# Performance work log

Hardware: AMD Instinct MI355X
Metric: run time of the kernel (lower is better)

## Reference

```python
import jax, jax.numpy as jnp
import numpy as np

N = 50000   # nodes
E = 800000  # edges
IN, HID, OUT = 128, 128, 64


def setup_inputs() -> dict:
    key = jax.random.key(0)
    ks = jax.random.split(key, 16)
    x = jax.random.normal(ks[0], (N, IN), dtype=jnp.float32)
    src = jax.random.randint(ks[1], (E,), 0, N, dtype=jnp.int32)
    dst = jax.random.randint(ks[2], (E,), 0, N, dtype=jnp.int32)
    s = 1.0 / np.sqrt(IN)
    W_self1 = jax.random.normal(ks[3], (IN, HID), dtype=jnp.float32) * s
    W_neigh1 = jax.random.normal(ks[4], (IN, HID), dtype=jnp.float32) * s
    b1 = jnp.zeros((HID,), dtype=jnp.float32)
    W_self2 = jax.random.normal(ks[5], (HID, HID), dtype=jnp.float32) * s
    W_neigh2 = jax.random.normal(ks[6], (HID, HID), dtype=jnp.float32) * s
    b2 = jnp.zeros((HID,), dtype=jnp.float32)
    W_self3 = jax.random.normal(ks[7], (HID, OUT), dtype=jnp.float32) * s
    W_neigh3 = jax.random.normal(ks[8], (HID, OUT), dtype=jnp.float32) * s
    b3 = jnp.zeros((OUT,), dtype=jnp.float32)
    # dropout(p=0.5) masks, pre-scaled by 1/(1-p)
    keep = 0.5
    mask1 = (jax.random.uniform(ks[9], (N, HID)) < keep).astype(jnp.float32) / keep
    mask2 = (jax.random.uniform(ks[10], (N, HID)) < keep).astype(jnp.float32) / keep
    return dict(x=x, src=src, dst=dst,
                W_self1=W_self1, W_neigh1=W_neigh1, b1=b1,
                W_self2=W_self2, W_neigh2=W_neigh2, b2=b2,
                W_self3=W_self3, W_neigh3=W_neigh3, b3=b3,
                mask1=mask1, mask2=mask2)


def _mean_agg(h, src, dst):
    # gather source features, segment-sum into destinations, divide by in-degree
    summed = jax.ops.segment_sum(h[src], dst, num_segments=N)  # [N, d]
    deg = jax.ops.segment_sum(jnp.ones((E,), dtype=h.dtype), dst, num_segments=N)
    return summed / jnp.maximum(deg, 1.0)[:, None]


def _sage_layer(h, src, dst, W_self, W_neigh, b):
    h_neigh = _mean_agg(h, src, dst)
    return h @ W_self + h_neigh @ W_neigh + b


def reference(x, src, dst, W_self1, W_neigh1, b1, W_self2, W_neigh2, b2,
              W_self3, W_neigh3, b3, mask1, mask2):
    h = _sage_layer(x, src, dst, W_self1, W_neigh1, b1)
    h = jax.nn.relu(h) * mask1
    h = _sage_layer(h, src, dst, W_self2, W_neigh2, b2)
    h = jax.nn.relu(h) * mask2
    h = _sage_layer(h, src, dst, W_self3, W_neigh3, b3)
    return h
```

## Files before the change

### kernel.cpp

```cpp
#include <hip/hip_runtime.h>
#include <hip/hip_bf16.h>

#define DIN  128
#define DHID 128
#define DOUT 64

#define EB   4096
#define CAPB 5120

typedef short short8 __attribute__((ext_vector_type(8)));
typedef float f32x4  __attribute__((ext_vector_type(4)));

__device__ __forceinline__ ushort f2bf(float f) {
    union { float f; uint u; } c; c.f = f;
    uint u = c.u;
    return (ushort)((u + 0x7fff + ((u >> 16) & 1)) >> 16);
}
__device__ __forceinline__ float bf2f(uint h16) {
    union { uint u; float f; } c; c.u = h16 << 16;
    return c.f;
}
__device__ __forceinline__ float sb8(uint u, int k) {
    return (float)((int)(u << (24 - 8 * k)) >> 24);
}

__device__ __forceinline__ void wprep_dev(const float* __restrict__ W,
                                          ushort* __restrict__ Wt, int OUT, int idx) {
    int nn = idx >> 7;
    int k  = idx & 127;
    Wt[idx] = f2bf(W[(size_t)k * OUT + nn]);
}

__global__ __launch_bounds__(256)
void megaprep(const int* __restrict__ src, const int* __restrict__ dst, int E, int fillB,
              int* __restrict__ bkt_cur, uint* __restrict__ pairs,
              const float* __restrict__ x, ushort* __restrict__ xb, int n4, int cvtB,
              const float* __restrict__ Ws1, const float* __restrict__ Wn1,
              const float* __restrict__ Ws2, const float* __restrict__ Wn2,
              const float* __restrict__ Ws3, const float* __restrict__ Wn3,
              ushort* __restrict__ Wst1, ushort* __restrict__ Wnt1,
              ushort* __restrict__ Wst2, ushort* __restrict__ Wnt2,
              ushort* __restrict__ Wst3, ushort* __restrict__ Wnt3) {
    __shared__ int c[256];
    __shared__ int startl[256];
    __shared__ int ofs[256];
    int b = blockIdx.x;
    const int t = threadIdx.x;
    if (b < fillB) {
        c[t] = 0;
        __syncthreads();
        const int base = b * EB;
        const int end = min(base + EB, E);
        for (int i = base + t; i < end; i += 256)
            atomicAdd(&c[dst[i] >> 8], 1);
        __syncthreads();
        int v = c[t];
        startl[t] = v ? (t * CAPB + atomicAdd(&bkt_cur[t], v)) : 0;
        ofs[t] = 0;
        __syncthreads();
        for (int i = base + t; i < end; i += 256) {
            int d = dst[i];
            int bb = d >> 8;
            int p = startl[bb] + atomicAdd(&ofs[bb], 1);
            pairs[p] = ((uint)src[i] << 8) | (uint)(d & 255);
        }
        return;
    }
    b -= fillB;
    if (b < cvtB) {
        int i = b * 256 + t;
        if (i < n4) {
            float4 v = ((const float4*)x)[i];
            ushort4 o;
            o.x = f2bf(v.x); o.y = f2bf(v.y); o.z = f2bf(v.z); o.w = f2bf(v.w);
            ((ushort4*)xb)[i] = o;
        }
        return;
    }
    b -= cvtB;
    if (b < 64)  { wprep_dev(Ws1, Wst1, 128, b * 256 + t); return; }
    b -= 64;
    if (b < 64)  { wprep_dev(Wn1, Wnt1, 128, b * 256 + t); return; }
    b -= 64;
    if (b < 64)  { wprep_dev(Ws2, Wst2, 128, b * 256 + t); return; }
    b -= 64;
    if (b < 64)  { wprep_dev(Wn2, Wnt2, 128, b * 256 + t); return; }
    b -= 64;
    if (b < 32)  { wprep_dev(Ws3, Wst3, 64, b * 256 + t); return; }
    b -= 32;
    wprep_dev(Wn3, Wnt3, 64, b * 256 + t);
}

__global__ __launch_bounds__(256)
void bucket_csr(const uint* __restrict__ pairs, const int* __restrict__ bkt_cur,
                int* __restrict__ row_ptr, int* __restrict__ deg,
                int* __restrict__ esrc, int N, int nbkt) {
    constexpr int CAP = 6144;
    __shared__ uint pl[CAP];
    __shared__ int cnt[256];
    __shared__ int rs[256];
    __shared__ int sc[256];
    const int bkt = blockIdx.x;
    const int t = threadIdx.x;
    const int ebase = bkt * CAPB;
    const int ecnt  = min(bkt_cur[bkt], CAPB);
    cnt[t] = 0;
    __syncthreads();
    const bool fits = (ecnt <= CAP);
    if (fits) {
        for (int i = t; i < ecnt; i += 256) {
            uint p = pairs[ebase + i];
            pl[i] = p;
            atomicAdd(&cnt[p & 255u], 1);
        }
    } else {
        for (int i = t; i < ecnt; i += 256)
            atomicAdd(&cnt[pairs[ebase + i] & 255u], 1);
    }
    __syncthreads();
    int own = cnt[t];
    sc[t] = own;
    __syncthreads();
    for (int o = 1; o < 256; o <<= 1) {
        int u = (t >= o) ? sc[t - o] : 0;
        __syncthreads();
        sc[t] += u;
        __syncthreads();
    }
    rs[t] = sc[t] - own;
    const int node = bkt * 256 + t;
    if (node < N) {
        row_ptr[node] = ebase + rs[t];
        deg[node] = own;
    }
    __syncthreads();
    if (fits) {
        for (int i = t; i < ecnt; i += 256) {
            uint p = pl[i];
            int pos = atomicAdd(&rs[p & 255u], 1);
            esrc[ebase + pos] = (int)(p >> 8);
        }
    } else {
        for (int i = t; i < ecnt; i += 256) {
            uint p = pairs[ebase + i];
            int pos = atomicAdd(&rs[p & 255u], 1);
            esrc[ebase + pos] = (int)(p >> 8);
        }
    }
}

template<int OUTW>
__global__ __launch_bounds__(256)
void sage_gemm(const ushort* __restrict__ Hb,
               const ushort* __restrict__ Wst,
               const ushort* __restrict__ Wnt,
               ushort* __restrict__ S,
               signed char* __restrict__ Gq,
               float* __restrict__ Gsc,
               int n) {
    constexpr int NT = OUTW / 16;
    __shared__ ushort Wl[2][OUTW * 128];

    const int tid  = threadIdx.x;
    const int lane = tid & 63;
    const int wave = tid >> 6;
    const int rg   = wave >> 1;
    const int isG  = wave & 1;
    const int m16  = lane & 15;
    const int kb   = lane >> 4;
    const int rbase = blockIdx.x * 64 + rg * 32;

    {
        const uint4* s4 = (const uint4*)Wst;
        const uint4* n4 = (const uint4*)Wnt;
        uint4* ls = (uint4*)&Wl[0][0];
        uint4* ln = (uint4*)&Wl[1][0];
#pragma unroll
        for (int j = tid; j < OUTW * 128 / 8; j += 256) {
            ls[j] = s4[j];
            ln[j] = n4[j];
        }
    }

    short8 a[2][4];
#pragma unroll
    for (int mt = 0; mt < 2; ++mt) {
        int arow = rbase + mt * 16 + m16;
        if (arow >= n) arow = n - 1;
        const ushort* __restrict__ Ap = &Hb[(size_t)arow * 128 + kb * 8];
#pragma unroll
        for (int c = 0; c < 4; ++c)
            a[mt][c] = *(const short8*)(Ap + c * 32);
    }

    __syncthreads();

    f32x4 acc[2][NT];
#pragma unroll
    for (int mt = 0; mt < 2; ++mt)
#pragma unroll
        for (int t = 0; t < NT; ++t) acc[mt][t] = (f32x4)(0.f);

    const ushort* __restrict__ Wp = &Wl[isG][0];
#pragma unroll
    for (int t = 0; t < NT; ++t) {
#pragma unroll
        for (int c = 0; c < 4; ++c) {
            short8 b = *(const short8*)&Wp[(t * 16 + m16) * 128 + c * 32 + kb * 8];
            acc[0][t] = __builtin_amdgcn_mfma_f32_16x16x32_bf16(a[0][c], b, acc[0][t], 0, 0, 0);
            acc[1][t] = __builtin_amdgcn_mfma_f32_16x16x32_bf16(a[1][c], b, acc[1][t], 0, 0, 0);
        }
    }

#pragma unroll
    for (int mt = 0; mt < 2; ++mt) {
        const int rb = rbase + mt * 16;
        if (!isG) {
#pragma unroll
            for (int r = 0; r < 4; ++r) {
                int row = rb + kb * 4 + r;
                if (row >= n) continue;
#pragma unroll
                for (int t = 0; t < NT; ++t)
                    S[(size_t)row * OUTW + t * 16 + m16] = f2bf(acc[mt][t][r]);
            }
        } else {
#pragma unroll
            for (int r = 0; r < 4; ++r) {
                float mx = 0.f;
#pragma unroll
                for (int t = 0; t < NT; ++t) mx = fmaxf(mx, fabsf(acc[mt][t][r]));
                mx = fmaxf(mx, __shfl_xor(mx, 1));
                mx = fmaxf(mx, __shfl_xor(mx, 2));
                mx = fmaxf(mx, __shfl_xor(mx, 4));
                mx = fmaxf(mx, __shfl_xor(mx, 8));
                int row = rb + kb * 4 + r;
                if (row >= n) continue;
                float inv = (mx > 0.f) ? 127.f / mx : 0.f;
                if (m16 == 0) Gsc[row] = mx * (1.f / 127.f);
#pragma unroll
                for (int t = 0; t < NT; ++t) {
                    int q = (int)rintf(acc[mt][t][r] * inv);
                    q = max(-127, min(127, q));
                    Gq[(size_t)row * OUTW + t * 16 + m16] = (signed char)q;
                }
            }
        }
    }
}

__device__ __forceinline__ void acc8(float* af, uint2 v, float sc) {
    af[0] += sc * sb8(v.x, 0); af[1] += sc * sb8(v.x, 1);
    af[2] += sc * sb8(v.x, 2); af[3] += sc * sb8(v.x, 3);
    af[4] += sc * sb8(v.y, 0); af[5] += sc * sb8(v.y, 1);
    af[6] += sc * sb8(v.y, 2); af[7] += sc * sb8(v.y, 3);
}
__device__ __forceinline__ void acc4(float* af, uint v, float sc) {
    af[0] += sc * sb8(v, 0); af[1] += sc * sb8(v, 1);
    af[2] += sc * sb8(v, 2); af[3] += sc * sb8(v, 3);
}

#define SPAN_CAP 1024

template<bool FINAL>
__global__ __launch_bounds__(256)
void sage_gather(const signed char* __restrict__ Gq, const float* __restrict__ Gsc,
                 const ushort* __restrict__ S, const float* __restrict__ bias,
                 const float* __restrict__ mask,
                 const int* __restrict__ row_ptr, const int* __restrict__ deg,
                 const int* __restrict__ esrc,
                 void* __restrict__ outv, int n) {
    constexpr int OUTW = FINAL ? 64 : 128;
    __shared__ int   idx_s[SPAN_CAP];
    __shared__ float sc_s[SPAN_CAP];

    const int tid  = threadIdx.x;
    const int lane = tid & 63;
    const int wave = tid >> 6;
    const int qw   = lane >> 4;
    const int l16  = lane & 15;
    const int base = blockIdx.x * 32;

    const int last   = min(base + 31, n - 1);
    const int span_s = row_ptr[base];
    const int span_e = row_ptr[last] + deg[last];
    const int len    = span_e - span_s;
    const bool staged = (len <= SPAN_CAP);
    if (staged) {
        for (int i = tid; i < len; i += 256) {
            int s_ = esrc[span_s + i];
            idx_s[i] = s_;
            sc_s[i] = Gsc[s_];
        }
    }
    __syncthreads();

#pragma unroll
    for (int j = 0; j < 2; ++j) {
        const int node = base + (wave * 4 + qw) * 2 + j;
        if (node >= n) continue;
        const int d = deg[node];
        const float inv = 1.f / fmaxf((float)d, 1.f);

        float af[8] = {0.f, 0.f, 0.f, 0.f, 0.f, 0.f, 0.f, 0.f};
        if (!FINAL) {
            const signed char* __restrict__ gp = Gq + l16 * 8;
            if (staged) {
                int i = row_ptr[node] - span_s, e = i + d;
                for (; i + 7 < e; i += 8) {
                    uint2 v[8]; float c[8];
#pragma unroll
                    for (int k = 0; k < 8; ++k) {
                        int ns = idx_s[i + k];
                        v[k] = *(const uint2*)&gp[(size_t)ns * 128];
                        c[k] = sc_s[i + k];
                    }
#pragma unroll
                    for (int k = 0; k < 8; ++k) acc8(af, v[k], c[k]);
                }
                for (; i < e; ++i) {
                    int ns = idx_s[i];
                    acc8(af, *(const uint2*)&gp[(size_t)ns * 128], sc_s[i]);
                }
            } else {
                int i = row_ptr[node], e = i + d;
                for (; i < e; ++i) {
                    int ns = esrc[i];
                    acc8(af, *(const uint2*)&gp[(size_t)ns * 128], Gsc[ns]);
                }
            }
            const int col0 = l16 * 8;
            uint4 sv = *(const uint4*)&S[(size_t)node * 128 + col0];
            float4 b0 = *(const float4*)&bias[col0];
            float4 b1 = *(const float4*)&bias[col0 + 4];
            float z[8];
            z[0] = bf2f(sv.x & 0xffffu) + af[0] * inv + b0.x;
            z[1] = bf2f(sv.x >> 16)     + af[1] * inv + b0.y;
            z[2] = bf2f(sv.y & 0xffffu) + af[2] * inv + b0.z;
            z[3] = bf2f(sv.y >> 16)     + af[3] * inv + b0.w;
            z[4] = bf2f(sv.z & 0xffffu) + af[4] * inv + b1.x;
            z[5] = bf2f(sv.z >> 16)     + af[5] * inv + b1.y;
            z[6] = bf2f(sv.w & 0xffffu) + af[6] * inv + b1.z;
            z[7] = bf2f(sv.w >> 16)     + af[7] * inv + b1.w;
            float4 m0 = *(const float4*)&mask[(size_t)node * 128 + col0];
            float4 m1 = *(const float4*)&mask[(size_t)node * 128 + col0 + 4];
            z[0] = fmaxf(z[0], 0.f) * m0.x; z[1] = fmaxf(z[1], 0.f) * m0.y;
            z[2] = fmaxf(z[2], 0.f) * m0.z; z[3] = fmaxf(z[3], 0.f) * m0.w;
            z[4] = fmaxf(z[4], 0.f) * m1.x; z[5] = fmaxf(z[5], 0.f) * m1.y;
            z[6] = fmaxf(z[6], 0.f) * m1.z; z[7] = fmaxf(z[7], 0.f) * m1.w;
            uint4 pk;
            pk.x = (uint)f2bf(z[0]) | ((uint)f2bf(z[1]) << 16);
            pk.y = (uint)f2bf(z[2]) | ((uint)f2bf(z[3]) << 16);
            pk.z = (uint)f2bf(z[4]) | ((uint)f2bf(z[5]) << 16);
            pk.w = (uint)f2bf(z[6]) | ((uint)f2bf(z[7]) << 16);
            *(uint4*)&((ushort*)outv)[(size_t)node * 128 + col0] = pk;
        } else {
            const signed char* __restrict__ gp = Gq + l16 * 4;
            if (staged) {
                int i = row_ptr[node] - span_s, e = i + d;
                for (; i + 7 < e; i += 8) {
                    uint v[8]; float c[8];
#pragma unroll
                    for (int k = 0; k < 8; ++k) {
                        int ns = idx_s[i + k];
                        v[k] = *(const uint*)&gp[(size_t)ns * 64];
                        c[k] = sc_s[i + k];
                    }
#pragma unroll
                    for (int k = 0; k < 8; ++k) acc4(af, v[k], c[k]);
                }
                for (; i < e; ++i) {
                    int ns = idx_s[i];
                    acc4(af, *(const uint*)&gp[(size_t)ns * 64], sc_s[i]);
                }
            } else {
                int i = row_ptr[node], e = i + d;
                for (; i < e; ++i) {
                    int ns = esrc[i];
                    acc4(af, *(const uint*)&gp[(size_t)ns * 64], Gsc[ns]);
                }
            }
            const int col0 = l16 * 4;
            uint2 sv = *(const uint2*)&S[(size_t)node * 64 + col0];
            float4 b0 = *(const float4*)&bias[col0];
            float4 z;
            z.x = bf2f(sv.x & 0xffffu) + af[0] * inv + b0.x;
            z.y = bf2f(sv.x >> 16)     + af[1] * inv + b0.y;
            z.z = bf2f(sv.y & 0xffffu) + af[2] * inv + b0.z;
            z.w = bf2f(sv.y >> 16)     + af[3] * inv + b0.w;
            *(float4*)&((float*)outv)[(size_t)node * 64 + col0] = z;
        }
    }
}

extern "C" void kernel_launch(void* const* d_in, const int* in_sizes, int n_in,
                              void* d_out, int out_size, void* d_ws, size_t ws_size,
                              hipStream_t stream) {
    const float* x   = (const float*)d_in[0];
    const int*   src = (const int*)d_in[1];
    const int*   dst = (const int*)d_in[2];
    const float* Ws1 = (const float*)d_in[3];
    const float* Wn1 = (const float*)d_in[4];
    const float* b1  = (const float*)d_in[5];
    const float* Ws2 = (const float*)d_in[6];
    const float* Wn2 = (const float*)d_in[7];
    const float* b2  = (const float*)d_in[8];
    const float* Ws3 = (const float*)d_in[9];
    const float* Wn3 = (const float*)d_in[10];
    const float* b3  = (const float*)d_in[11];
    const float* mask1 = (const float*)d_in[12];
    const float* mask2 = (const float*)d_in[13];
    float* out = (float*)d_out;

    const int N = in_sizes[0] / DIN;
    const int E = in_sizes[1];
    const int nbkt = (N + 255) >> 8;

    char* ws = (char*)d_ws;
    int* bkt_cur  = (int*)ws;
    int* row_ptr  = bkt_cur + 256;
    int* deg      = row_ptr + N;
    int* esrc     = deg + N;
    size_t off = ((size_t)(256 + 2 * N + nbkt * CAPB) * sizeof(int) + 255) & ~(size_t)255;
    uint* pairs  = (uint*)(ws + off);    off += (size_t)nbkt * CAPB * 4;
    ushort* xb   = (ushort*)(ws + off);  off += (size_t)N * 128 * 2;
    ushort* h1b  = (ushort*)(ws + off);  off += (size_t)N * 128 * 2;
    ushort* h2b  = (ushort*)(ws + off);  off += (size_t)N * 128 * 2;
    ushort* S    = (ushort*)(ws + off);  off += (size_t)N * 128 * 2;
    signed char* Gq = (signed char*)(ws + off); off += (size_t)N * 128;
    float* Gsc   = (float*)(ws + off);   off += (size_t)N * 4;
    ushort* Wst1 = (ushort*)(ws + off);  off += 128 * 128 * 2;
    ushort* Wnt1 = (ushort*)(ws + off);  off += 128 * 128 * 2;
    ushort* Wst2 = (ushort*)(ws + off);  off += 128 * 128 * 2;
    ushort* Wnt2 = (ushort*)(ws + off);  off += 128 * 128 * 2;
    ushort* Wst3 = (ushort*)(ws + off);  off += 64 * 128 * 2;
    ushort* Wnt3 = (ushort*)(ws + off);  off += 64 * 128 * 2;

    const int n4 = N * 128 / 4;
    const int cvtB = (n4 + 255) / 256;
    const int fillB = (E + EB - 1) / EB;

    hipMemsetAsync(bkt_cur, 0, 256 * sizeof(int), stream);
    megaprep<<<fillB + cvtB + 4 * 64 + 2 * 32, 256, 0, stream>>>(
        src, dst, E, fillB, bkt_cur, pairs,
        x, xb, n4, cvtB,
        Ws1, Wn1, Ws2, Wn2, Ws3, Wn3,
        Wst1, Wnt1, Wst2, Wnt2, Wst3, Wnt3);

    bucket_csr<<<nbkt, 256, 0, stream>>>(pairs, bkt_cur, row_ptr, deg, esrc, N, nbkt);

    const int gemmB = (N + 63) / 64;
    const int gathB = (N + 31) / 32;

    sage_gemm<128><<<gemmB, 256, 0, stream>>>(xb, Wst1, Wnt1, S, Gq, Gsc, N);
    sage_gather<false><<<gathB, 256, 0, stream>>>(Gq, Gsc, S, b1, mask1, row_ptr, deg, esrc, h1b, N);
    sage_gemm<128><<<gemmB, 256, 0, stream>>>(h1b, Wst2, Wnt2, S, Gq, Gsc, N);
    sage_gather<false><<<gathB, 256, 0, stream>>>(Gq, Gsc, S, b2, mask2, row_ptr, deg, esrc, h2b, N);
    sage_gemm<64><<<gemmB, 256, 0, stream>>>(h2b, Wst3, Wnt3, S, Gq, Gsc, N);
    sage_gather<true><<<gathB, 256, 0, stream>>>(Gq, Gsc, S, b3, nullptr, row_ptr, deg, esrc, out, N);
}
```

Baseline: 296.5 us.

## Fuse self-term GEMM into gather kernel and drop bf16 S buffer round trip

The self projection h@W_self moves from the GEMM kernel into the gather kernel. Each gather block computes its 32 rows with MFMA into shared-memory float tiles, so the separate S buffer is no longer written and re-read through global memory. The GEMM kernel now computes only the neighbor projection and its int8 quantization, one 16-row tile per wave. The self term is now kept in fp32 instead of rounded to bf16. The trade-off is more shared memory and extra weight loads per gather block, which may lower occupancy. The bucket_csr kernel also drops its fallback path for oversized buckets and always stages pairs in shared memory.

```diff
diff --git a/kernel.cpp b/kernel.cpp
--- a/kernel.cpp
+++ b/kernel.cpp
@@ -106,16 +106,10 @@
     const int ecnt  = min(bkt_cur[bkt], CAPB);
     cnt[t] = 0;
     __syncthreads();
-    const bool fits = (ecnt <= CAP);
-    if (fits) {
-        for (int i = t; i < ecnt; i += 256) {
-            uint p = pairs[ebase + i];
-            pl[i] = p;
-            atomicAdd(&cnt[p & 255u], 1);
-        }
-    } else {
-        for (int i = t; i < ecnt; i += 256)
-            atomicAdd(&cnt[pairs[ebase + i] & 255u], 1);
+    for (int i = t; i < ecnt; i += 256) {
+        uint p = pairs[ebase + i];
+        pl[i] = p;
+        atomicAdd(&cnt[p & 255u], 1);
     }
     __syncthreads();
     int own = cnt[t];
@@ -134,117 +128,80 @@
         deg[node] = own;
     }
     __syncthreads();
-    if (fits) {
-        for (int i = t; i < ecnt; i += 256) {
-            uint p = pl[i];
-            int pos = atomicAdd(&rs[p & 255u], 1);
-            esrc[ebase + pos] = (int)(p >> 8);
-        }
-    } else {
-        for (int i = t; i < ecnt; i += 256) {
-            uint p = pairs[ebase + i];
-            int pos = atomicAdd(&rs[p & 255u], 1);
-            esrc[ebase + pos] = (int)(p >> 8);
-        }
+    for (int i = t; i < ecnt; i += 256) {
+        uint p = pl[i];
+        int pos = atomicAdd(&rs[p & 255u], 1);
+        esrc[ebase + pos] = (int)(p >> 8);
     }
 }
 
 template<int OUTW>
 __global__ __launch_bounds__(256)
-void sage_gemm(const ushort* __restrict__ Hb,
-               const ushort* __restrict__ Wst,
-               const ushort* __restrict__ Wnt,
-               ushort* __restrict__ S,
-               signed char* __restrict__ Gq,
-               float* __restrict__ Gsc,
-               int n) {
+void gemm_G(const ushort* __restrict__ Hb,
+            const ushort* __restrict__ Wnt,
+            signed char* __restrict__ Gq,
+            float* __restrict__ Gsc,
+            int n) {
     constexpr int NT = OUTW / 16;
-    __shared__ ushort Wl[2][OUTW * 128];
+    __shared__ ushort Wl[OUTW * 128];
 
     const int tid  = threadIdx.x;
     const int lane = tid & 63;
     const int wave = tid >> 6;
-    const int rg   = wave >> 1;
-    const int isG  = wave & 1;
     const int m16  = lane & 15;
     const int kb   = lane >> 4;
-    const int rbase = blockIdx.x * 64 + rg * 32;
+    const int rbase = blockIdx.x * 64 + wave * 16;
 
     {
-        const uint4* s4 = (const uint4*)Wst;
         const uint4* n4 = (const uint4*)Wnt;
-        uint4* ls = (uint4*)&Wl[0][0];
-        uint4* ln = (uint4*)&Wl[1][0];
-#pragma unroll
-        for (int j = tid; j < OUTW * 128 / 8; j += 256) {
-            ls[j] = s4[j];
+        uint4* ln = (uint4*)&Wl[0];
+#pragma unroll
+        for (int j = tid; j < OUTW * 128 / 8; j += 256)
             ln[j] = n4[j];
-        }
-    }
-
-    short8 a[2][4];
-#pragma unroll
-    for (int mt = 0; mt < 2; ++mt) {
-        int arow = rbase + mt * 16 + m16;
-        if (arow >= n) arow = n - 1;
+    }
+
+    short8 a[4];
+    {
+        int arow = rbase + m16; if (arow >= n) arow = n - 1;
         const ushort* __restrict__ Ap = &Hb[(size_t)arow * 128 + kb * 8];
 #pragma unroll
         for (int c = 0; c < 4; ++c)
-            a[mt][c] = *(const short8*)(Ap + c * 32);
-    }
-
-    __syncthreads();
-
-    f32x4 acc[2][NT];
-#pragma unroll
-    for (int mt = 0; mt < 2; ++mt)
-#pragma unroll
-        for (int t = 0; t < NT; ++t) acc[mt][t] = (f32x4)(0.f);
-
-    const ushort* __restrict__ Wp = &Wl[isG][0];
+            a[c] = *(const short8*)(Ap + c * 32);
+    }
+
+    __syncthreads();
+
+    f32x4 acc[NT];
+#pragma unroll
+    for (int t = 0; t < NT; ++t) acc[t] = (f32x4)(0.f);
+
 #pragma unroll
     for (int t = 0; t < NT; ++t) {
 #pragma unroll
         for (int c = 0; c < 4; ++c) {
-            short8 b = *(const short8*)&Wp[(t * 16 + m16) * 128 + c * 32 + kb * 8];
-            acc[0][t] = __builtin_amdgcn_mfma_f32_16x16x32_bf16(a[0][c], b, acc[0][t], 0, 0, 0);
-            acc[1][t] = __builtin_amdgcn_mfma_f32_16x16x32_bf16(a[1][c], b, acc[1][t], 0, 0, 0);
-        }
-    }
-
-#pragma unroll
-    for (int mt = 0; mt < 2; ++mt) {
-        const int rb = rbase + mt * 16;
-        if (!isG) {
-#pragma unroll
-            for (int r = 0; r < 4; ++r) {
-                int row = rb + kb * 4 + r;
-                if (row >= n) continue;
-#pragma unroll
-                for (int t = 0; t < NT; ++t)
-                    S[(size_t)row * OUTW + t * 16 + m16] = f2bf(acc[mt][t][r]);
-            }
-        } else {
-#pragma unroll
-            for (int r = 0; r < 4; ++r) {
-                float mx = 0.f;
-#pragma unroll
-                for (int t = 0; t < NT; ++t) mx = fmaxf(mx, fabsf(acc[mt][t][r]));
-                mx = fmaxf(mx, __shfl_xor(mx, 1));
-                mx = fmaxf(mx, __shfl_xor(mx, 2));
-                mx = fmaxf(mx, __shfl_xor(mx, 4));
-                mx = fmaxf(mx, __shfl_xor(mx, 8));
-                int row = rb + kb * 4 + r;
-                if (row >= n) continue;
-                float inv = (mx > 0.f) ? 127.f / mx : 0.f;
-                if (m16 == 0) Gsc[row] = mx * (1.f / 127.f);
-#pragma unroll
-                for (int t = 0; t < NT; ++t) {
-                    int q = (int)rintf(acc[mt][t][r] * inv);
-                    q = max(-127, min(127, q));
-                    Gq[(size_t)row * OUTW + t * 16 + m16] = (signed char)q;
-                }
-            }
+            short8 b = *(const short8*)&Wl[(t * 16 + m16) * 128 + c * 32 + kb * 8];
+            acc[t] = __builtin_amdgcn_mfma_f32_16x16x32_bf16(a[c], b, acc[t], 0, 0, 0);
+        }
+    }
+
+#pragma unroll
+    for (int r = 0; r < 4; ++r) {
+        float mx = 0.f;
+#pragma unroll
+        for (int t = 0; t < NT; ++t) mx = fmaxf(mx, fabsf(acc[t][r]));
+        mx = fmaxf(mx, __shfl_xor(mx, 1));
+        mx = fmaxf(mx, __shfl_xor(mx, 2));
+        mx = fmaxf(mx, __shfl_xor(mx, 4));
+        mx = fmaxf(mx, __shfl_xor(mx, 8));
+        int row = rbase + kb * 4 + r;
+        if (row >= n) continue;
+        float inv = (mx > 0.f) ? 127.f / mx : 0.f;
+        if (m16 == 0) Gsc[row] = mx * (1.f / 127.f);
+#pragma unroll
+        for (int t = 0; t < NT; ++t) {
+            int q = (int)rintf(acc[t][r] * inv);
+            q = max(-127, min(127, q));
+            Gq[(size_t)row * OUTW + t * 16 + m16] = (signed char)q;
         }
     }
 }
@@ -264,15 +221,19 @@
 
 template<bool FINAL>
 __global__ __launch_bounds__(256)
-void sage_gather(const signed char* __restrict__ Gq, const float* __restrict__ Gsc,
-                 const ushort* __restrict__ S, const float* __restrict__ bias,
-                 const float* __restrict__ mask,
-                 const int* __restrict__ row_ptr, const int* __restrict__ deg,
-                 const int* __restrict__ esrc,
-                 void* __restrict__ outv, int n) {
+void gather_S(const ushort* __restrict__ Hb,
+              const ushort* __restrict__ Wst,
+              const signed char* __restrict__ Gq, const float* __restrict__ Gsc,
+              const float* __restrict__ bias, const float* __restrict__ mask,
+              const int* __restrict__ row_ptr, const int* __restrict__ deg,
+              const int* __restrict__ esrc,
+              void* __restrict__ outv, int n) {
     constexpr int OUTW = FINAL ? 64 : 128;
-    __shared__ int   idx_s[SPAN_CAP];
-    __shared__ float sc_s[SPAN_CAP];
+    constexpr int SP   = OUTW + 4;
+    __shared__ ushort Wl[OUTW * 128];
+    __shared__ float  Sl[32 * SP];
+    __shared__ int    idx_s[SPAN_CAP];
+    __shared__ float  sc_s[SPAN_CAP];
 
     const int tid  = threadIdx.x;
     const int lane = tid & 63;
@@ -280,6 +241,27 @@
     const int qw   = lane >> 4;
     const int l16  = lane & 15;
     const int base = blockIdx.x * 32;
+    const int m16  = l16;
+    const int kb   = qw;
+
+    const int mt = wave & 1;
+    const int nq = wave >> 1;
+    short8 a[4];
+    {
+        int arow = base + mt * 16 + m16; if (arow >= n) arow = n - 1;
+        const ushort* __restrict__ Ap = &Hb[(size_t)arow * 128 + kb * 8];
+#pragma unroll
+        for (int c = 0; c < 4; ++c)
+            a[c] = *(const short8*)(Ap + c * 32);
+    }
+
+    {
+        const uint4* s4 = (const uint4*)Wst;
+        uint4* ls = (uint4*)&Wl[0];
+#pragma unroll
+        for (int j = tid; j < OUTW * 128 / 8; j += 256)
+            ls[j] = s4[j];
+    }
 
     const int last   = min(base + 31, n - 1);
     const int span_s = row_ptr[base];
@@ -295,15 +277,37 @@
     }
     __syncthreads();
 
+    {
+        constexpr int TPW = FINAL ? 2 : 4;
+        f32x4 acc[TPW];
+#pragma unroll
+        for (int t = 0; t < TPW; ++t) acc[t] = (f32x4)(0.f);
+#pragma unroll
+        for (int t = 0; t < TPW; ++t) {
+#pragma unroll
+            for (int c = 0; c < 4; ++c) {
+                short8 b = *(const short8*)&Wl[(nq * TPW * 16 + t * 16 + m16) * 128 + c * 32 + kb * 8];
+                acc[t] = __builtin_amdgcn_mfma_f32_16x16x32_bf16(a[c], b, acc[t], 0, 0, 0);
+            }
+        }
+#pragma unroll
+        for (int t = 0; t < TPW; ++t)
+#pragma unroll
+            for (int r = 0; r < 4; ++r)
+                Sl[(mt * 16 + kb * 4 + r) * SP + nq * TPW * 16 + t * 16 + m16] = acc[t][r];
+    }
+    __syncthreads();
+
 #pragma unroll
     for (int j = 0; j < 2; ++j) {
         const int node = base + (wave * 4 + qw) * 2 + j;
         if (node >= n) continue;
+        const int ln = node - base;
         const int d = deg[node];
         const float inv = 1.f / fmaxf((float)d, 1.f);
 
-        float af[8] = {0.f, 0.f, 0.f, 0.f, 0.f, 0.f, 0.f, 0.f};
         if (!FINAL) {
+            float af[8] = {0.f, 0.f, 0.f, 0.f, 0.f, 0.f, 0.f, 0.f};
             const signed char* __restrict__ gp = Gq + l16 * 8;
             if (staged) {
                 int i = row_ptr[node] - span_s, e = i + d;
@@ -330,18 +334,19 @@
                 }
             }
             const int col0 = l16 * 8;
-            uint4 sv = *(const uint4*)&S[(size_t)node * 128 + col0];
+            float4 s0 = *(const float4*)&Sl[ln * SP + col0];
+            float4 s1 = *(const float4*)&Sl[ln * SP + col0 + 4];
             float4 b0 = *(const float4*)&bias[col0];
             float4 b1 = *(const float4*)&bias[col0 + 4];
             float z[8];
-            z[0] = bf2f(sv.x & 0xffffu) + af[0] * inv + b0.x;
-            z[1] = bf2f(sv.x >> 16)     + af[1] * inv + b0.y;
-            z[2] = bf2f(sv.y & 0xffffu) + af[2] * inv + b0.z;
-            z[3] = bf2f(sv.y >> 16)     + af[3] * inv + b0.w;
-            z[4] = bf2f(sv.z & 0xffffu) + af[4] * inv + b1.x;
-            z[5] = bf2f(sv.z >> 16)     + af[5] * inv + b1.y;
-            z[6] = bf2f(sv.w & 0xffffu) + af[6] * inv + b1.z;
-            z[7] = bf2f(sv.w >> 16)     + af[7] * inv + b1.w;
+            z[0] = s0.x + af[0] * inv + b0.x;
+            z[1] = s0.y + af[1] * inv + b0.y;
+            z[2] = s0.z + af[2] * inv + b0.z;
+            z[3] = s0.w + af[3] * inv + b0.w;
+            z[4] = s1.x + af[4] * inv + b1.x;
+            z[5] = s1.y + af[5] * inv + b1.y;
+            z[6] = s1.z + af[6] * inv + b1.z;
+            z[7] = s1.w + af[7] * inv + b1.w;
             float4 m0 = *(const float4*)&mask[(size_t)node * 128 + col0];
             float4 m1 = *(const float4*)&mask[(size_t)node * 128 + col0 + 4];
             z[0] = fmaxf(z[0], 0.f) * m0.x; z[1] = fmaxf(z[1], 0.f) * m0.y;
@@ -355,6 +360,7 @@
             pk.w = (uint)f2bf(z[6]) | ((uint)f2bf(z[7]) << 16);
             *(uint4*)&((ushort*)outv)[(size_t)node * 128 + col0] = pk;
         } else {
+            float af[4] = {0.f, 0.f, 0.f, 0.f};
             const signed char* __restrict__ gp = Gq + l16 * 4;
             if (staged) {
                 int i = row_ptr[node] - span_s, e = i + d;
@@ -381,13 +387,13 @@
                 }
             }
             const int col0 = l16 * 4;
-            uint2 sv = *(const uint2*)&S[(size_t)node * 64 + col0];
+            float4 s0 = *(const float4*)&Sl[ln * SP + col0];
             float4 b0 = *(const float4*)&bias[col0];
             float4 z;
-            z.x = bf2f(sv.x & 0xffffu) + af[0] * inv + b0.x;
-            z.y = bf2f(sv.x >> 16)     + af[1] * inv + b0.y;
-            z.z = bf2f(sv.y & 0xffffu) + af[2] * inv + b0.z;
-            z.w = bf2f(sv.y >> 16)     + af[3] * inv + b0.w;
+            z.x = s0.x + af[0] * inv + b0.x;
+            z.y = s0.y + af[1] * inv + b0.y;
+            z.z = s0.z + af[2] * inv + b0.z;
+            z.w = s0.w + af[3] * inv + b0.w;
             *(float4*)&((float*)outv)[(size_t)node * 64 + col0] = z;
         }
     }
@@ -426,7 +432,6 @@
     ushort* xb   = (ushort*)(ws + off);  off += (size_t)N * 128 * 2;
     ushort* h1b  = (ushort*)(ws + off);  off += (size_t)N * 128 * 2;
     ushort* h2b  = (ushort*)(ws + off);  off += (size_t)N * 128 * 2;
-    ushort* S    = (ushort*)(ws + off);  off += (size_t)N * 128 * 2;
     signed char* Gq = (signed char*)(ws + off); off += (size_t)N * 128;
     float* Gsc   = (float*)(ws + off);   off += (size_t)N * 4;
     ushort* Wst1 = (ushort*)(ws + off);  off += 128 * 128 * 2;
@@ -452,10 +457,10 @@
     const int gemmB = (N + 63) / 64;
     const int gathB = (N + 31) / 32;
 
-    sage_gemm<128><<<gemmB, 256, 0, stream>>>(xb, Wst1, Wnt1, S, Gq, Gsc, N);
-    sage_gather<false><<<gathB, 256, 0, stream>>>(Gq, Gsc, S, b1, mask1, row_ptr, deg, esrc, h1b, N);
-    sage_gemm<128><<<gemmB, 256, 0, stream>>>(h1b, Wst2, Wnt2, S, Gq, Gsc, N);
-    sage_gather<false><<<gathB, 256, 0, stream>>>(Gq, Gsc, S, b2, mask2, row_ptr, deg, esrc, h2b, N);
-    sage_gemm<64><<<gemmB, 256, 0, stream>>>(h2b, Wst3, Wnt3, S, Gq, Gsc, N);
-    sage_gather<true><<<gathB, 256, 0, stream>>>(Gq, Gsc, S, b3, nullptr, row_ptr, deg, esrc, out, N);
-}
+    gemm_G<128><<<gemmB, 256, 0, stream>>>(xb, Wnt1, Gq, Gsc, N);
+    gather_S<false><<<gathB, 256, 0, stream>>>(xb, Wst1, Gq, Gsc, b1, mask1, row_ptr, deg, esrc, h1b, N);
+    gemm_G<128><<<gemmB, 256, 0, stream>>>(h1b, Wnt2, Gq, Gsc, N);
+    gather_S<false><<<gathB, 256, 0, stream>>>(h1b, Wst2, Gq, Gsc, b2, mask2, row_ptr, deg, esrc, h2b, N);
+    gemm_G<64><<<gemmB, 256, 0, stream>>>(h2b, Wnt3, Gq, Gsc, N);
+    gather_S<true><<<gathB, 256, 0, stream>>>(h2b, Wst3, Gq, Gsc, b3, nullptr, row_ptr, deg, esrc, out, N);
+}
```

New measurement: 347.1 us. +17.0%, slower.
